# Performance work log

Measured on AMD Instinct MI355X. Metric: run time of the kernel, lower is better.

## Reference

```python
import jax, jax.numpy as jnp
import numpy as np

N = 4096        # number of sparse voxel tokens (single sequence)
C = 1024        # channels
H = 16          # num_heads
D = C // H      # head_dim = 64
FREQ_DIM = D // 2 // 3   # 10 rotary freqs per spatial axis
PAD = D // 2 - 3 * FREQ_DIM  # 2 identity-padded complex pairs


def setup_inputs() -> dict:
    key = jax.random.key(0)
    ks = jax.random.split(key, 6)
    s_in = 1.0 / np.sqrt(C)
    x = jax.random.normal(ks[0], (N, C), jnp.float32)
    coords = jax.random.randint(ks[1], (N, 3), 0, 64, dtype=jnp.int32)
    W_qkv = jax.random.normal(ks[2], (C, 3 * C), jnp.float32) * s_in
    b_qkv = jnp.zeros((3 * C,), jnp.float32)
    gamma_q = jnp.ones((H, D), jnp.float32)
    gamma_k = jnp.ones((H, D), jnp.float32)
    W_out = jax.random.normal(ks[3], (C, C), jnp.float32) * s_in
    b_out = jnp.zeros((C,), jnp.float32)
    return {"x": x, "coords": coords, "W_qkv": W_qkv, "b_qkv": b_qkv,
            "gamma_q": gamma_q, "gamma_k": gamma_k, "W_out": W_out, "b_out": b_out}


def _rms_norm(t, gamma):
    # F.normalize(x, dim=-1) * gamma * sqrt(D), computed in fp32
    t = t.astype(jnp.float32)
    nrm = jnp.maximum(jnp.linalg.norm(t, axis=-1, keepdims=True), 1e-12)
    return (t / nrm) * gamma * np.float32(np.sqrt(D))


def _rope_phases(coords):
    # freqs: rope_freq[0] / rope_freq[1]**(i/freq_dim)
    freqs = 1.0 / (10000.0 ** (jnp.arange(FREQ_DIM, dtype=jnp.float32) / FREQ_DIM))
    ph = coords.astype(jnp.float32).reshape(-1)[:, None] * freqs   # [N*3, FREQ_DIM]
    ph = ph.reshape(N, 3 * FREQ_DIM)
    # pad with zero-phase (identity rotation) to head_dim//2
    cos = jnp.concatenate([jnp.cos(ph), jnp.ones((N, PAD), jnp.float32)], axis=-1)
    sin = jnp.concatenate([jnp.sin(ph), jnp.zeros((N, PAD), jnp.float32)], axis=-1)
    return cos, sin


def _rope_apply(t, cos, sin):
    # complex rotation on consecutive pairs of the head dim
    tr = t.reshape(N, H, D // 2, 2)
    t0, t1 = tr[..., 0], tr[..., 1]
    c, s = cos[:, None, :], sin[:, None, :]
    o0 = t0 * c - t1 * s
    o1 = t0 * s + t1 * c
    return jnp.stack([o0, o1], axis=-1).reshape(N, H, D)


def reference(x, coords, W_qkv, b_qkv, gamma_q, gamma_k, W_out, b_out):
    qkv = (x @ W_qkv + b_qkv).reshape(N, 3, H, D)
    q, k, v = qkv[:, 0], qkv[:, 1], qkv[:, 2]
    q = _rms_norm(q, gamma_q)
    k = _rms_norm(k, gamma_k)
    cos, sin = _rope_phases(coords)
    q = _rope_apply(q, cos, sin)
    k = _rope_apply(k, cos, sin)
    scores = jnp.einsum('nhd,mhd->hnm', q, k) / np.float32(np.sqrt(D))
    attn = jax.nn.softmax(scores, axis=-1)
    h = jnp.einsum('hnm,mhd->nhd', attn, v).reshape(N, C)
    return h @ W_out + b_out
```

## Files before the change

kernel.cpp:

```cpp
#include <hip/hip_runtime.h>

#define DEVI __device__ __forceinline__

typedef __attribute__((ext_vector_type(8))) short bf16x8;
typedef __attribute__((ext_vector_type(4))) float f32x4;
typedef __attribute__((ext_vector_type(16))) float f32x16;

DEVI ushort f2bf(float f) {
  union { float f; unsigned u; } v; v.f = f;
  unsigned u = v.u;
  unsigned r = (u + 0x7FFFu + ((u >> 16) & 1u)) >> 16;
  return (ushort)r;
}
DEVI float bf2f(ushort h) {
  union { unsigned u; float f; } v; v.u = ((unsigned)h) << 16;
  return v.f;
}
DEVI unsigned pkbf(float lo, float hi) {
  unsigned r;
  asm("v_cvt_pk_bf16_f32 %0, %1, %2" : "=v"(r) : "v"(lo), "v"(hi));
  return r;
}
DEVI float exp2v(float x) {
#if __has_builtin(__builtin_amdgcn_exp2f)
  return __builtin_amdgcn_exp2f(x);
#else
  return exp2f(x);
#endif
}

DEVI void gload_lds16(const ushort* g, ushort* l) {
  __builtin_amdgcn_global_load_lds((const __attribute__((address_space(1))) void*)g,
                                   (__attribute__((address_space(3))) void*)l, 16, 0, 0);
}

__global__ __launch_bounds__(256) void cast_x(const float* __restrict__ in,
                                              ushort* __restrict__ out, int n4) {
  int i = blockIdx.x * blockDim.x + threadIdx.x;
  if (i < n4) {
    const float4 v = ((const float4*)in)[i];
    uint2 o;
    o.x = (unsigned)f2bf(v.x) | ((unsigned)f2bf(v.y) << 16);
    o.y = (unsigned)f2bf(v.z) | ((unsigned)f2bf(v.w) << 16);
    ((uint2*)out)[i] = o;
  }
}

__global__ __launch_bounds__(256) void transpose_cast(const float* __restrict__ in,
                                                      ushort* __restrict__ out,
                                                      int R, int Cc) {
  __shared__ ushort tile[64][65];
  const int t = threadIdx.x;
  const int r0 = blockIdx.y * 64, c0 = blockIdx.x * 64;
  for (int i = 0; i < 16; ++i) {
    int rr = i * 4 + (t >> 6), cc = t & 63;
    tile[rr][cc] = f2bf(in[(size_t)(r0 + rr) * Cc + c0 + cc]);
  }
  __syncthreads();
  for (int i = 0; i < 16; ++i) {
    int cc = i * 4 + (t >> 6), rr = t & 63;
    out[(size_t)(c0 + cc) * R + r0 + rr] = tile[rr][cc];
  }
}

template<int EPI>
__global__ __launch_bounds__(256) void gemm_bt(const ushort* __restrict__ A,
                                               const ushort* __restrict__ Bt,
                                               const float* __restrict__ bias,
                                               void* __restrict__ outp,
                                               int M, int Nn, int K) {
  __shared__ ushort As[128 * 32];
  __shared__ ushort Bs[128 * 32];
  const int tid = threadIdx.x;
  const int w = tid >> 6, l = tid & 63;
  const int m0 = blockIdx.y * 128, n0 = blockIdx.x * 128;
  const int wm = (w >> 1) * 64, wn = (w & 1) * 64;
  const int lc = l & 15, lg = l >> 4;

  f32x4 acc[4][4];
  for (int i = 0; i < 4; ++i)
    for (int j = 0; j < 4; ++j) acc[i][j] = (f32x4){0.f, 0.f, 0.f, 0.f};

  const int srow = w * 32 + (l >> 2);
  const int scol = (l & 3) * 8;
  const ushort* gA = A + (size_t)(m0 + srow) * K + scol;
  const ushort* gB = Bt + (size_t)(n0 + srow) * K + scol;

  for (int k0 = 0; k0 < K; k0 += 32) {
    gload_lds16(gA + k0,                 As + (w * 32 + 0) * 32);
    gload_lds16(gA + k0 + (size_t)16 * K, As + (w * 32 + 16) * 32);
    gload_lds16(gB + k0,                 Bs + (w * 32 + 0) * 32);
    gload_lds16(gB + k0 + (size_t)16 * K, Bs + (w * 32 + 16) * 32);
    __syncthreads();
    bf16x8 af[4], bfr[4];
    for (int mi = 0; mi < 4; ++mi)
      af[mi] = *(const bf16x8*)(As + (wm + mi * 16 + lc) * 32 + lg * 8);
    for (int ni = 0; ni < 4; ++ni)
      bfr[ni] = *(const bf16x8*)(Bs + (wn + ni * 16 + lc) * 32 + lg * 8);
    for (int mi = 0; mi < 4; ++mi)
      for (int ni = 0; ni < 4; ++ni)
        acc[mi][ni] = __builtin_amdgcn_mfma_f32_16x16x32_bf16(af[mi], bfr[ni], acc[mi][ni], 0, 0, 0);
    __syncthreads();
  }

  const int lr = lg * 4;
  if constexpr (EPI == 1) {
    float* O = (float*)outp;
    for (int ni = 0; ni < 4; ++ni) {
      int col = n0 + wn + ni * 16 + lc;
      float bv = bias[col];
      for (int mi = 0; mi < 4; ++mi)
        for (int r = 0; r < 4; ++r)
          O[(size_t)(m0 + wm + mi * 16 + lr + r) * Nn + col] = acc[mi][ni][r] + bv;
    }
  } else {
    ushort* O = (ushort*)outp;
    for (int ni = 0; ni < 4; ++ni) {
      int col = n0 + wn + ni * 16 + lc;
      float bv = bias[col];
      int grp = col >> 10;
      int hh = (col >> 6) & 15;
      int dd = col & 63;
      if (grp < 2) {
        size_t base = (size_t)grp * (16 * 4096 * 64) + (size_t)hh * (4096 * 64) + dd;
        for (int mi = 0; mi < 4; ++mi)
          for (int r = 0; r < 4; ++r) {
            int row = m0 + wm + mi * 16 + lr + r;
            O[base + (size_t)row * 64] = f2bf(acc[mi][ni][r] + bv);
          }
      } else {
        size_t base = (size_t)2 * (16 * 4096 * 64) + ((size_t)hh * 64 + dd) * 4096;
        for (int mi = 0; mi < 4; ++mi)
          for (int r = 0; r < 4; ++r) {
            int row = m0 + wm + mi * 16 + lr + r;
            O[base + row] = f2bf(acc[mi][ni][r] + bv);
          }
      }
    }
  }
}

DEVI void nr_one(ushort* B, const float* g, size_t base, int h, int l16,
                 float c0a, float s0a, float c1a, float s1a, float extra) {
  unsigned u0 = *(const unsigned*)(B + base + 2 * l16);
  unsigned u1 = *(const unsigned*)(B + base + 32 + 2 * l16);
  float t00 = bf2f((ushort)u0), t01 = bf2f((ushort)(u0 >> 16));
  float t10 = bf2f((ushort)u1), t11 = bf2f((ushort)(u1 >> 16));
  float ss = t00 * t00 + t01 * t01 + t10 * t10 + t11 * t11;
  for (int d = 1; d < 16; d <<= 1) ss += __shfl_xor(ss, d, 16);
  float scl = 8.f / fmaxf(sqrtf(ss), 1e-12f);
  scl *= extra;
  float g00 = g[h * 64 + 2 * l16], g01 = g[h * 64 + 2 * l16 + 1];
  float g10 = g[h * 64 + 32 + 2 * l16], g11 = g[h * 64 + 33 + 2 * l16];
  float q00 = t00 * scl * g00, q01 = t01 * scl * g01;
  float q10 = t10 * scl * g10, q11 = t11 * scl * g11;
  float o00 = q00 * c0a - q01 * s0a, o01 = q00 * s0a + q01 * c0a;
  float o10 = q10 * c1a - q11 * s1a, o11 = q10 * s1a + q11 * c1a;
  *(unsigned*)(B + base + 2 * l16) = (unsigned)f2bf(o00) | ((unsigned)f2bf(o01) << 16);
  *(unsigned*)(B + base + 32 + 2 * l16) = (unsigned)f2bf(o10) | ((unsigned)f2bf(o11) << 16);
}

__global__ __launch_bounds__(256) void norm_rope(ushort* __restrict__ Qb,
                                                 ushort* __restrict__ Kb,
                                                 const int* __restrict__ coords,
                                                 const float* __restrict__ gq,
                                                 const float* __restrict__ gk) {
  const int n = blockIdx.x, t = threadIdx.x;
  const int h = t >> 4, l16 = t & 15;
  const float L2_10K_D10 = 1.3287712379549449f;
  float c0a, s0a, c1a, s1a;
  {
    int p = l16;
    int j = p / 10, fi = p - j * 10;
    float freq = exp2f(-(float)fi * L2_10K_D10);
    float ang = (float)coords[n * 3 + j] * freq;
    c0a = cosf(ang); s0a = sinf(ang);
  }
  {
    int p = l16 + 16;
    if (p < 30) {
      int j = p / 10, fi = p - j * 10;
      float freq = exp2f(-(float)fi * L2_10K_D10);
      float ang = (float)coords[n * 3 + j] * freq;
      c1a = cosf(ang); s1a = sinf(ang);
    } else { c1a = 1.f; s1a = 0.f; }
  }
  const size_t base = ((size_t)h * 4096 + n) * 64;
  nr_one(Qb, gq, base, h, l16, c0a, s0a, c1a, s1a, 0.125f * 1.4426950408889634f);
  nr_one(Kb, gk, base, h, l16, c0a, s0a, c1a, s1a, 1.0f);
}

DEVI void attn_step(const bf16x8 (&ck)[8], const bf16x8 (&cv)[8], const bf16x8 (&qf)[4],
                    f32x16& o0, f32x16& o1, float& mr, float& lsum) {
  f32x16 s0, s1;
#pragma unroll
  for (int r = 0; r < 16; ++r) { s0[r] = 0.f; s1[r] = 0.f; }
#pragma unroll
  for (int c = 0; c < 4; ++c) {
    s0 = __builtin_amdgcn_mfma_f32_32x32x16_bf16(ck[c],     qf[c], s0, 0, 0, 0);
    s1 = __builtin_amdgcn_mfma_f32_32x32x16_bf16(ck[c + 4], qf[c], s1, 0, 0, 0);
  }

  float m8[8];
#pragma unroll
  for (int r = 0; r < 8; ++r)
    m8[r] = fmaxf(fmaxf(s0[r], s0[r + 8]), fmaxf(s1[r], s1[r + 8]));
  float tm = fmaxf(fmaxf(fmaxf(m8[0], m8[1]), fmaxf(m8[2], m8[3])),
                   fmaxf(fmaxf(m8[4], m8[5]), fmaxf(m8[6], m8[7])));
  tm = fmaxf(tm, __shfl_xor(tm, 32));

  if (!__all(tm <= mr + 8.f)) {
    float mnew = fmaxf(mr, tm);
    float corr = exp2v(mr - mnew);
    lsum *= corr;
#pragma unroll
    for (int r = 0; r < 16; ++r) { o0[r] *= corr; o1[r] *= corr; }
    mr = mnew;
  }
  float rsa = 0.f, rsb = 0.f, rsc = 0.f, rsd = 0.f;
#pragma unroll
  for (int r = 0; r < 16; r += 4) {
    s0[r]     = exp2v(s0[r]     - mr); rsa += s0[r];
    s0[r + 1] = exp2v(s0[r + 1] - mr); rsb += s0[r + 1];
    s0[r + 2] = exp2v(s0[r + 2] - mr); rsc += s0[r + 2];
    s0[r + 3] = exp2v(s0[r + 3] - mr); rsd += s0[r + 3];
  }
#pragma unroll
  for (int r = 0; r < 16; r += 4) {
    s1[r]     = exp2v(s1[r]     - mr); rsa += s1[r];
    s1[r + 1] = exp2v(s1[r + 1] - mr); rsb += s1[r + 1];
    s1[r + 2] = exp2v(s1[r + 2] - mr); rsc += s1[r + 2];
    s1[r + 3] = exp2v(s1[r + 3] - mr); rsd += s1[r + 3];
  }
  float rs = (rsa + rsb) + (rsc + rsd);
  rs += __shfl_xor(rs, 32);
  lsum += rs;

  union { unsigned u[4]; bf16x8 v; } pb[4];
  {
    auto r0 = __builtin_amdgcn_permlane32_swap(pkbf(s0[0], s0[1]), pkbf(s0[4], s0[5]), false, false);
    auto r1 = __builtin_amdgcn_permlane32_swap(pkbf(s0[2], s0[3]), pkbf(s0[6], s0[7]), false, false);
    pb[0].u[0] = r0[0]; pb[0].u[1] = r1[0]; pb[0].u[2] = r0[1]; pb[0].u[3] = r1[1];
    auto r2 = __builtin_amdgcn_permlane32_swap(pkbf(s0[8], s0[9]), pkbf(s0[12], s0[13]), false, false);
    auto r3 = __builtin_amdgcn_permlane32_swap(pkbf(s0[10], s0[11]), pkbf(s0[14], s0[15]), false, false);
    pb[1].u[0] = r2[0]; pb[1].u[1] = r3[0]; pb[1].u[2] = r2[1]; pb[1].u[3] = r3[1];
    auto r4 = __builtin_amdgcn_permlane32_swap(pkbf(s1[0], s1[1]), pkbf(s1[4], s1[5]), false, false);
    auto r5 = __builtin_amdgcn_permlane32_swap(pkbf(s1[2], s1[3]), pkbf(s1[6], s1[7]), false, false);
    pb[2].u[0] = r4[0]; pb[2].u[1] = r5[0]; pb[2].u[2] = r4[1]; pb[2].u[3] = r5[1];
    auto r6 = __builtin_amdgcn_permlane32_swap(pkbf(s1[8], s1[9]), pkbf(s1[12], s1[13]), false, false);
    auto r7 = __builtin_amdgcn_permlane32_swap(pkbf(s1[10], s1[11]), pkbf(s1[14], s1[15]), false, false);
    pb[3].u[0] = r6[0]; pb[3].u[1] = r7[0]; pb[3].u[2] = r6[1]; pb[3].u[3] = r7[1];
  }

#pragma unroll
  for (int c = 0; c < 4; ++c) {
    o0 = __builtin_amdgcn_mfma_f32_32x32x16_bf16(cv[c],     pb[c].v, o0, 0, 0, 0);
    o1 = __builtin_amdgcn_mfma_f32_32x32x16_bf16(cv[c + 4], pb[c].v, o1, 0, 0, 0);
  }
}

__global__ __launch_bounds__(256, 2) void attn_fwd(const ushort* __restrict__ Qb,
                                                   const ushort* __restrict__ Kb,
                                                   const ushort* __restrict__ Vt,
                                                   ushort* __restrict__ attnb) {
  __shared__ ushort Ks[2][4096];
  __shared__ ushort Vs[2][4096];

  const int flat = blockIdx.x + (blockIdx.y << 5);
  const int swz = (flat & 7) * 64 + (flat >> 3);
  const int bx = swz & 31, h = swz >> 5;

  const int l = threadIdx.x & 63, w = threadIdx.x >> 6;
  const int q = l & 31, hi = l >> 5;
  const int q0 = bx * 128 + w * 32;

  const ushort* qrow = Qb + ((size_t)h * 4096 + q0 + q) * 64 + hi * 8;
  bf16x8 qf[4];
#pragma unroll
  for (int c = 0; c < 4; ++c) qf[c] = *(const bf16x8*)(qrow + 16 * c);

  f32x16 o0, o1;
#pragma unroll
  for (int r = 0; r < 16; ++r) { o0[r] = 0.f; o1[r] = 0.f; }
  float mr = -1e30f, lsum = 0.f;

  const ushort* gK = Kb + ((size_t)h * 4096 + l) * 64 + 2 * w * 8;
  const ushort* gV = Vt + ((size_t)h * 64 + l) * 4096 + 2 * w * 8;

  ushort* Kc = &Ks[0][0]; ushort* Vc = &Vs[0][0];
  ushort* Kn = &Ks[1][0]; ushort* Vn = &Vs[1][0];

  gload_lds16(gK, Kc + 2 * w * 512);
  gload_lds16(gK + 8, Kc + (2 * w + 1) * 512);
  gload_lds16(gV, Vc + 2 * w * 512);
  gload_lds16(gV + 8, Vc + (2 * w + 1) * 512);
  asm volatile("s_waitcnt vmcnt(0)" ::: "memory");
  __builtin_amdgcn_s_barrier();
  __builtin_amdgcn_sched_barrier(0);

  const int lbase = hi * 512 + q * 8;
  for (int t = 0; t < 63; ++t) {
    const ushort* sK = gK + (size_t)(t + 1) * 64 * 64;
    const ushort* sV = gV + (t + 1) * 64;
    gload_lds16(sK, Kn + 2 * w * 512);
    gload_lds16(sK + 8, Kn + (2 * w + 1) * 512);
    gload_lds16(sV, Vn + 2 * w * 512);
    gload_lds16(sV + 8, Vn + (2 * w + 1) * 512);

    bf16x8 k[8], v[8];
#pragma unroll
    for (int c = 0; c < 4; ++c) {
      k[c]     = *(const bf16x8*)(Kc + lbase + c * 1024);
      k[c + 4] = *(const bf16x8*)(Kc + lbase + c * 1024 + 256);
      v[c]     = *(const bf16x8*)(Vc + lbase + c * 1024);
      v[c + 4] = *(const bf16x8*)(Vc + lbase + c * 1024 + 256);
    }
    __builtin_amdgcn_s_setprio(1);
    attn_step(k, v, qf, o0, o1, mr, lsum);
    __builtin_amdgcn_s_setprio(0);

    asm volatile("s_waitcnt vmcnt(0) lgkmcnt(0)" ::: "memory");
    __builtin_amdgcn_s_barrier();
    __builtin_amdgcn_sched_barrier(0);
    ushort* tp;
    tp = Kc; Kc = Kn; Kn = tp;
    tp = Vc; Vc = Vn; Vn = tp;
  }
  {
    bf16x8 k[8], v[8];
#pragma unroll
    for (int c = 0; c < 4; ++c) {
      k[c]     = *(const bf16x8*)(Kc + lbase + c * 1024);
      k[c + 4] = *(const bf16x8*)(Kc + lbase + c * 1024 + 256);
      v[c]     = *(const bf16x8*)(Vc + lbase + c * 1024);
      v[c + 4] = *(const bf16x8*)(Vc + lbase + c * 1024 + 256);
    }
    attn_step(k, v, qf, o0, o1, mr, lsum);
  }

  const float inv = 1.f / lsum;
  ushort* orow = attnb + (size_t)(q0 + q) * 1024 + h * 64;
#pragma unroll
  for (int dt = 0; dt < 2; ++dt) {
    const f32x16& oo = dt ? o1 : o0;
#pragma unroll
    for (int g = 0; g < 4; ++g)
#pragma unroll
      for (int p2 = 0; p2 < 2; ++p2) {
        int r = g * 4 + p2 * 2;
        unsigned pk = pkbf(oo[r] * inv, oo[r + 1] * inv);
        *(unsigned*)(orow + dt * 32 + g * 8 + 4 * hi + p2 * 2) = pk;
      }
  }
}

extern "C" void kernel_launch(void* const* d_in, const int* in_sizes, int n_in,
                              void* d_out, int out_size, void* d_ws, size_t ws_size,
                              hipStream_t stream) {
  const float* x      = (const float*)d_in[0];
  const int*   coords = (const int*)d_in[1];
  const float* W_qkv  = (const float*)d_in[2];
  const float* b_qkv  = (const float*)d_in[3];
  const float* gq     = (const float*)d_in[4];
  const float* gk     = (const float*)d_in[5];
  const float* W_out  = (const float*)d_in[6];
  const float* b_out  = (const float*)d_in[7];
  float* out = (float*)d_out;

  char* ws = (char*)d_ws;
  ushort* xb    = (ushort*)(ws);
  ushort* wtqkv = (ushort*)(ws + (8u << 20));
  ushort* wtout = (ushort*)(ws + (14u << 20));
  ushort* Qb    = (ushort*)(ws + (16u << 20));
  ushort* Kb    = (ushort*)(ws + (24u << 20));
  ushort* Vt    = (ushort*)(ws + (32u << 20));
  ushort* attnb = (ushort*)(ws + (40u << 20));

  cast_x<<<4096, 256, 0, stream>>>(x, xb, 4096 * 1024 / 4);
  transpose_cast<<<dim3(48, 16), 256, 0, stream>>>(W_qkv, wtqkv, 1024, 3072);
  transpose_cast<<<dim3(16, 16), 256, 0, stream>>>(W_out, wtout, 1024, 1024);
  gemm_bt<0><<<dim3(24, 32), 256, 0, stream>>>(xb, wtqkv, b_qkv, (void*)Qb, 4096, 3072, 1024);
  norm_rope<<<4096, 256, 0, stream>>>(Qb, Kb, coords, gq, gk);
  attn_fwd<<<dim3(32, 16), 256, 0, stream>>>(Qb, Kb, Vt, attnb);
  gemm_bt<1><<<dim3(8, 32), 256, 0, stream>>>(attnb, wtout, b_out, (void*)out, 4096, 1024, 1024);
}
```

Before: 184.5 us.

## Triple-buffer K/V tiles in attention with two-ahead prefetch

Moves the attention kernel from double to triple buffering of K/V shared-memory tiles and prefetches two tiles ahead. Each iteration waits only for the oldest outstanding loads (vmcnt(4)) instead of draining all memory traffic, so global load latency is hidden behind more compute. The cost is 50% more LDS per block (48KB vs 32KB), which could affect the 2-blocks-per-CU occupancy target. The lgkmcnt wait is also dropped, and the safety of reusing a buffer now rests on the barrier ordering.

```diff
diff --git a/kernel.cpp b/kernel.cpp
--- a/kernel.cpp
+++ b/kernel.cpp
@@ -263,8 +263,8 @@
                                                    const ushort* __restrict__ Kb,
                                                    const ushort* __restrict__ Vt,
                                                    ushort* __restrict__ attnb) {
-  __shared__ ushort Ks[2][4096];
-  __shared__ ushort Vs[2][4096];
+  __shared__ ushort Ks[3][4096];
+  __shared__ ushort Vs[3][4096];
 
   const int flat = blockIdx.x + (blockIdx.y << 5);
   const int swz = (flat & 7) * 64 + (flat >> 3);
@@ -287,26 +287,32 @@
   const ushort* gK = Kb + ((size_t)h * 4096 + l) * 64 + 2 * w * 8;
   const ushort* gV = Vt + ((size_t)h * 64 + l) * 4096 + 2 * w * 8;
 
-  ushort* Kc = &Ks[0][0]; ushort* Vc = &Vs[0][0];
-  ushort* Kn = &Ks[1][0]; ushort* Vn = &Vs[1][0];
-
-  gload_lds16(gK, Kc + 2 * w * 512);
-  gload_lds16(gK + 8, Kc + (2 * w + 1) * 512);
-  gload_lds16(gV, Vc + 2 * w * 512);
-  gload_lds16(gV + 8, Vc + (2 * w + 1) * 512);
-  asm volatile("s_waitcnt vmcnt(0)" ::: "memory");
+  gload_lds16(gK,          &Ks[0][2 * w * 512]);
+  gload_lds16(gK + 8,      &Ks[0][(2 * w + 1) * 512]);
+  gload_lds16(gV,          &Vs[0][2 * w * 512]);
+  gload_lds16(gV + 8,      &Vs[0][(2 * w + 1) * 512]);
+  gload_lds16(gK + 4096,     &Ks[1][2 * w * 512]);
+  gload_lds16(gK + 4096 + 8, &Ks[1][(2 * w + 1) * 512]);
+  gload_lds16(gV + 64,       &Vs[1][2 * w * 512]);
+  gload_lds16(gV + 64 + 8,   &Vs[1][(2 * w + 1) * 512]);
+  asm volatile("s_waitcnt vmcnt(4)" ::: "memory");
   __builtin_amdgcn_s_barrier();
   __builtin_amdgcn_sched_barrier(0);
 
   const int lbase = hi * 512 + q * 8;
-  for (int t = 0; t < 63; ++t) {
-    const ushort* sK = gK + (size_t)(t + 1) * 64 * 64;
-    const ushort* sV = gV + (t + 1) * 64;
-    gload_lds16(sK, Kn + 2 * w * 512);
-    gload_lds16(sK + 8, Kn + (2 * w + 1) * 512);
-    gload_lds16(sV, Vn + 2 * w * 512);
-    gload_lds16(sV + 8, Vn + (2 * w + 1) * 512);
-
+  int cur = 0;
+  for (int t = 0; t < 64; ++t) {
+    int nx2 = cur + 2; nx2 = nx2 >= 3 ? nx2 - 3 : nx2;
+    if (t + 2 < 64) {
+      const ushort* sK = gK + (size_t)(t + 2) * 4096;
+      const ushort* sV = gV + (t + 2) * 64;
+      gload_lds16(sK,     &Ks[nx2][2 * w * 512]);
+      gload_lds16(sK + 8, &Ks[nx2][(2 * w + 1) * 512]);
+      gload_lds16(sV,     &Vs[nx2][2 * w * 512]);
+      gload_lds16(sV + 8, &Vs[nx2][(2 * w + 1) * 512]);
+    }
+    const ushort* Kc = &Ks[cur][0];
+    const ushort* Vc = &Vs[cur][0];
     bf16x8 k[8], v[8];
 #pragma unroll
     for (int c = 0; c < 4; ++c) {
@@ -318,24 +324,13 @@
     __builtin_amdgcn_s_setprio(1);
     attn_step(k, v, qf, o0, o1, mr, lsum);
     __builtin_amdgcn_s_setprio(0);
-
-    asm volatile("s_waitcnt vmcnt(0) lgkmcnt(0)" ::: "memory");
-    __builtin_amdgcn_s_barrier();
-    __builtin_amdgcn_sched_barrier(0);
-    ushort* tp;
-    tp = Kc; Kc = Kn; Kn = tp;
-    tp = Vc; Vc = Vn; Vn = tp;
-  }
-  {
-    bf16x8 k[8], v[8];
-#pragma unroll
-    for (int c = 0; c < 4; ++c) {
-      k[c]     = *(const bf16x8*)(Kc + lbase + c * 1024);
-      k[c + 4] = *(const bf16x8*)(Kc + lbase + c * 1024 + 256);
-      v[c]     = *(const bf16x8*)(Vc + lbase + c * 1024);
-      v[c + 4] = *(const bf16x8*)(Vc + lbase + c * 1024 + 256);
-    }
-    attn_step(k, v, qf, o0, o1, mr, lsum);
+    if (t < 63) {
+      if (t < 61) asm volatile("s_waitcnt vmcnt(4)" ::: "memory");
+      else        asm volatile("s_waitcnt vmcnt(0)" ::: "memory");
+      __builtin_amdgcn_s_barrier();
+      __builtin_amdgcn_sched_barrier(0);
+    }
+    cur = cur + 1 == 3 ? 0 : cur + 1;
   }
 
   const float inv = 1.f / lsum;
```

Result: slower. 195.2 us (+5.8%).
